# Performance work log

Hardware: AMD Instinct MI355X
Metric: run time of the kernel (lower is better)

## Reference

```python
import jax, jax.numpy as jnp
import numpy as np

B, CIN, COUT, TD, H, W = 32, 128, 128, 192, 64, 64
PH = PW = 8
HEADS, DEPTH, E, K, TASKS = 4, 2, 4, 2, 9
MLPH = int(2.0 * TD)


def _ln(x, g, b, eps=1e-5):
    m = jnp.mean(x, -1, keepdims=True)
    v = jnp.var(x, -1, keepdims=True)
    return (x - m) * jax.lax.rsqrt(v + eps) * g + b


def _conv(x, w):
    return jax.lax.conv_general_dilated(x, w, (1, 1), 'SAME',
        dimension_numbers=('NCHW', 'OIHW', 'NCHW'))


def _bn_act(x, g, b):
    y = g[None, :, None, None] * x + b[None, :, None, None]
    return jax.nn.silu(y)


def setup_inputs() -> dict:
    key = jax.random.key(0)
    ks = iter(jax.random.split(key, 40))
    def nrm(shape, s=0.02):
        return jax.random.normal(next(ks), shape, jnp.float32) * s
    return {
        'x': jax.random.normal(next(ks), (B, CIN, H, W), jnp.float32),
        'w_kxk': nrm((CIN, CIN, 3, 3)), 'bn1_g': jnp.ones((CIN,)), 'bn1_b': jnp.zeros((CIN,)),
        'w_1x1': nrm((TD, CIN)),
        'gate_w': nrm((TASKS, TD, E)),
        'moe_w1': nrm((E, TD, TD)), 'moe_b1': jnp.zeros((E, TD)),
        'moe_w2': nrm((E, TD, TD)), 'moe_b2': jnp.zeros((E, TD)),
        'ln1_g': jnp.ones((DEPTH, TD)), 'ln1_b': jnp.zeros((DEPTH, TD)),
        'qkv_w': nrm((DEPTH, TD, 3 * TD)), 'qkv_b': jnp.zeros((DEPTH, 3 * TD)),
        'proj_w': nrm((DEPTH, TD, TD)), 'proj_b': jnp.zeros((DEPTH, TD)),
        'ln2_g': jnp.ones((DEPTH, TD)), 'ln2_b': jnp.zeros((DEPTH, TD)),
        'fc1_w': nrm((DEPTH, TD, MLPH)), 'fc1_b': jnp.zeros((DEPTH, MLPH)),
        'fc2_w': nrm((DEPTH, MLPH, TD)), 'fc2_b': jnp.zeros((DEPTH, TD)),
        'nrm_g': jnp.ones((TD,)), 'nrm_b': jnp.zeros((TD,)),
        'w_proj': nrm((COUT, TD)), 'bn2_g': jnp.ones((COUT,)), 'bn2_b': jnp.zeros((COUT,)),
        'w_fus': nrm((COUT, CIN + COUT, 3, 3)), 'bn3_g': jnp.ones((COUT,)), 'bn3_b': jnp.zeros((COUT,)),
        'task_bh': 3,
    }


def reference(x, w_kxk, bn1_g, bn1_b, w_1x1, gate_w, moe_w1, moe_b1, moe_w2, moe_b2,
              ln1_g, ln1_b, qkv_w, qkv_b, proj_w, proj_b, ln2_g, ln2_b,
              fc1_w, fc1_b, fc2_w, fc2_b, nrm_g, nrm_b,
              w_proj, bn2_g, bn2_b, w_fus, bn3_g, bn3_b, task_bh):
    shortcut = x
    h = _bn_act(_conv(x, w_kxk), bn1_g, bn1_b)              # conv_kxk + BN + SiLU
    h = jnp.einsum('bchw,tc->bthw', h, w_1x1)               # conv_1x1 (no bias)
    Bh, C, Hh, Wh = h.shape                                 # C == TD
    nph, npw = Hh // PH, Wh // PW
    NP, PA = nph * npw, PH * PW
    # patchify: [B,C,H,W] -> [B*PA, NP, C]
    t = h.reshape(Bh * C * nph, PH, npw, PW)
    t = jnp.swapaxes(t, 1, 2).reshape(Bh, C, NP, PA)
    t = jnp.swapaxes(t, 1, 3).reshape(Bh * PA, NP, C)
    # TaskMoE: task-conditioned top-k routing
    N, S, D = t.shape
    tok = t.reshape(N * S, D)
    logits = tok @ gate_w[task_bh]                          # [T,E]
    probs = jax.nn.softmax(logits, -1)
    topv, topi = jax.lax.top_k(probs, K)
    gates = topv / jnp.sum(topv, -1, keepdims=True)
    dense = jnp.zeros_like(probs)
    for j in range(K):
        dense = dense + jax.nn.one_hot(topi[:, j], E, dtype=probs.dtype) * gates[:, j:j + 1]
    out = jnp.zeros_like(tok)
    for e in range(E):
        he = jax.nn.gelu(tok @ moe_w1[e] + moe_b1[e], approximate=False)
        out = out + dense[:, e:e + 1] * (he @ moe_w2[e] + moe_b2[e])
    importance = jnp.mean(probs, 0)
    load = jnp.mean((dense > 0).astype(probs.dtype), 0)
    moe_loss = E * jnp.sum(importance * load)
    t = out.reshape(N, S, D)
    # transformer blocks
    hd = D // HEADS
    scale = hd ** -0.5
    for l in range(DEPTH):
        y = _ln(t, ln1_g[l], ln1_b[l])
        qkv = (y @ qkv_w[l] + qkv_b[l]).reshape(N, S, 3, HEADS, hd)
        q, k_, v = qkv[:, :, 0], qkv[:, :, 1], qkv[:, :, 2]
        att = jax.nn.softmax(jnp.einsum('nqhd,nkhd->nhqk', q, k_) * scale, -1)
        y = jnp.einsum('nhqk,nkhd->nqhd', att, v).reshape(N, S, D)
        t = t + (y @ proj_w[l] + proj_b[l])
        y = _ln(t, ln2_g[l], ln2_b[l])
        y = jax.nn.gelu(y @ fc1_w[l] + fc1_b[l], approximate=False)
        t = t + (y @ fc2_w[l] + fc2_b[l])
    t = _ln(t, nrm_g, nrm_b)
    # unpatchify: [B*PA, NP, D] -> [B, D, H, W]
    u = t.reshape(Bh, PA, NP, D)
    u = jnp.swapaxes(u, 1, 3).reshape(Bh * D * nph, npw, PH, PW)
    u = jnp.swapaxes(u, 1, 2).reshape(Bh, D, nph * PH, npw * PW)
    p = _bn_act(jnp.einsum('bchw,oc->bohw', u, w_proj), bn2_g, bn2_b)  # conv_proj
    f = _bn_act(_conv(jnp.concatenate([shortcut, p], 1), w_fus), bn3_g, bn3_b)
    return (f, moe_loss)
```

## Files before the change

kernel.cpp:

```cpp
#include <hip/hip_runtime.h>
#include <hip/hip_bf16.h>
#include <cmath>

typedef __hip_bfloat16 bf16;
typedef __attribute__((ext_vector_type(8))) short short8;
typedef __attribute__((ext_vector_type(4))) float float4v;

__device__ __forceinline__ float b2f(bf16 v) { return __bfloat162float(v); }
__device__ __forceinline__ bf16  f2b(float v) { return __float2bfloat16(v); }
__device__ __forceinline__ float bfr(unsigned int u) { union { float f; unsigned int i; } c; c.i = u << 16; return c.f; }
__device__ __forceinline__ void ld4(const float* p, float* o) {
    float4 q = *(const float4*)p; o[0]=q.x; o[1]=q.y; o[2]=q.z; o[3]=q.w;
}
__device__ __forceinline__ void ld4(const bf16* p, float* o) {
    const uint2 q = *(const uint2*)p;
    o[0] = bfr(q.x & 0xffffu); o[1] = bfr(q.x >> 16);
    o[2] = bfr(q.y & 0xffffu); o[3] = bfr(q.y >> 16);
}
template <typename T>
__device__ __forceinline__ void ld8(const T* p, float* o) { ld4(p, o); ld4(p + 4, o + 4); }
__device__ __forceinline__ float ldv(const float* p) { return *p; }
__device__ __forceinline__ float ldv(const bf16* p)  { return b2f(*p); }
__device__ __forceinline__ void  stv(float* p, float v) { *p = v; }
__device__ __forceinline__ void  stv(bf16* p, float v)  { *p = f2b(v); }

__device__ __forceinline__ float siluf(float x) { return x / (1.f + expf(-x)); }
__device__ __forceinline__ float geluf(float x) { return 0.5f * x * (1.f + erff(x * 0.70710678118654752f)); }

__global__ __launch_bounds__(256) void k_prep(
    const float* __restrict__ src, bf16* __restrict__ dst, int K, int N, int nmat)
{
    const int per = K * N;
    const int total = per * nmat;
    const int NT = N >> 4;
    for (int idx = blockIdx.x * 256 + threadIdx.x; idx < total; idx += gridDim.x * 256) {
        int m = idx / per;
        int rem = idx - m * per;
        int k = rem / N, n = rem - k * N;
        int off = ((k >> 5) * NT + (n >> 4)) * 512 + (((k >> 3) & 3) * 16 + (n & 15)) * 8 + (k & 7);
        dst[(size_t)m * per + off] = f2b(src[idx]);
    }
}

__global__ __launch_bounds__(256) void k_prep_t(
    const float* __restrict__ src, bf16* __restrict__ dst, int N, int K)
{
    const int total = N * K;
    const int NT = N >> 4;
    for (int idx = blockIdx.x * 256 + threadIdx.x; idx < total; idx += gridDim.x * 256) {
        int n = idx / K, k = idx - n * K;
        int off = ((k >> 5) * NT + (n >> 4)) * 512 + (((k >> 3) & 3) * 16 + (n & 15)) * 8 + (k & 7);
        dst[off] = f2b(src[idx]);
    }
}

__global__ __launch_bounds__(256) void k_prep_conv(
    const float* __restrict__ src, bf16* __restrict__ dst, int Cin, int Cout)
{
    const int total = Cout * Cin * 9;
    const int NT = Cout >> 4;
    for (int idx = blockIdx.x * 256 + threadIdx.x; idx < total; idx += gridDim.x * 256) {
        int oc = idx / (Cin * 9);
        int rem = idx - oc * (Cin * 9);
        int ic = rem / 9, tap = rem - ic * 9;
        int off = tap * (Cin * Cout)
                + ((ic >> 5) * NT + (oc >> 4)) * 512
                + (((ic >> 3) & 3) * 16 + (oc & 15)) * 8 + (ic & 7);
        dst[off] = f2b(src[idx]);
    }
}

__global__ __launch_bounds__(256) void k_tohwc(const float* __restrict__ x, bf16* __restrict__ xh)
{
    __shared__ bf16 L[64][136];
    const int br = blockIdx.x;
    const int b = br >> 6, y = br & 63;
    for (int idx = threadIdx.x; idx < 8192; idx += 256) {
        int ch = idx >> 6, xc = idx & 63;
        L[xc][ch] = f2b(x[(((size_t)b * 128 + ch) * 64 + y) * 64 + xc]);
    }
    __syncthreads();
    for (int idx = threadIdx.x; idx < 1024; idx += 256) {
        int px = idx >> 4, q = idx & 15;
        *(short8*)(void*)(xh + ((size_t)br * 64 + px) * 128 + q * 8) =
            *(const short8*)(const void*)(&L[px][q * 8]);
    }
}

__global__ __launch_bounds__(256) void k_conv1_mfma(
    const bf16* __restrict__ xh, const bf16* __restrict__ wf,
    const float* __restrict__ gamma, const float* __restrict__ beta,
    bf16* __restrict__ h1h)
{
    __shared__ __align__(16) bf16 outL[64][136];
    const int br = blockIdx.x;
    const int b = br >> 6, y = br & 63;
    const int lane = threadIdx.x & 63, w = threadIdx.x >> 6;
    const int m0 = w * 16, kg = lane >> 4, ln16 = lane & 15;
    float4v acc[8];
    #pragma unroll
    for (int i = 0; i < 8; ++i) acc[i] = (float4v)0.f;
    #pragma unroll
    for (int tap = 0; tap < 9; ++tap) {
        const int ky = tap / 3 - 1, kx = tap % 3 - 1;
        const int yy = y + ky;
        if (yy < 0 || yy > 63) continue;
        const int px = m0 + ln16 + kx;
        const bool valid = (px >= 0) && (px < 64);
        const bf16* wt = wf + tap * 16384;
        #pragma unroll
        for (int kc = 0; kc < 4; ++kc) {
            short8 a = {0, 0, 0, 0, 0, 0, 0, 0};
            if (valid)
                a = *(const short8*)(const void*)(xh + (((size_t)(b * 64 + yy) * 64 + px) * 128) + kc * 32 + kg * 8);
            const bf16* wb = wt + (kc * 8) * 512 + lane * 8;
            #pragma unroll
            for (int nt = 0; nt < 8; ++nt) {
                short8 bfrag = *(const short8*)(const void*)(wb + nt * 512);
                acc[nt] = __builtin_amdgcn_mfma_f32_16x16x32_bf16(a, bfrag, acc[nt], 0, 0, 0);
            }
        }
    }
    #pragma unroll
    for (int nt = 0; nt < 8; ++nt) {
        int c = nt * 16 + ln16;
        float g = gamma[c], be = beta[c];
        #pragma unroll
        for (int r = 0; r < 4; ++r)
            outL[m0 + kg * 4 + r][c] = f2b(siluf(g * acc[nt][r] + be));
    }
    __syncthreads();
    for (int idx = threadIdx.x; idx < 1024; idx += 256) {
        int px = idx >> 4, q = idx & 15;
        *(short8*)(void*)(h1h + ((size_t)br * 64 + px) * 128 + q * 8) =
            *(const short8*)(const void*)(&outL[px][q * 8]);
    }
}

__global__ __launch_bounds__(256) void k_convf_mfma(
    const bf16* __restrict__ xh, const bf16* __restrict__ ph,
    const bf16* __restrict__ wf,
    const float* __restrict__ gamma, const float* __restrict__ beta,
    float* __restrict__ out)
{
    __shared__ float outF[64][129];
    const int br = blockIdx.x;
    const int b = br >> 6, y = br & 63;
    const int lane = threadIdx.x & 63, w = threadIdx.x >> 6;
    const int m0 = w * 16, kg = lane >> 4, ln16 = lane & 15;
    float4v acc[8];
    #pragma unroll
    for (int i = 0; i < 8; ++i) acc[i] = (float4v)0.f;
    #pragma unroll
    for (int tap = 0; tap < 9; ++tap) {
        const int ky = tap / 3 - 1, kx = tap % 3 - 1;
        const int yy = y + ky;
        if (yy < 0 || yy > 63) continue;
        const int px = m0 + ln16 + kx;
        const bool valid = (px >= 0) && (px < 64);
        const size_t rowoff = ((size_t)(b * 64 + yy) * 64 + px) * 128;
        const bf16* wt = wf + tap * 32768;
        #pragma unroll
        for (int kc = 0; kc < 8; ++kc) {
            const bf16* src = (kc < 4) ? xh : ph;
            short8 a = {0, 0, 0, 0, 0, 0, 0, 0};
            if (valid)
                a = *(const short8*)(const void*)(src + rowoff + (kc & 3) * 32 + kg * 8);
            const bf16* wb = wt + (kc * 8) * 512 + lane * 8;
            #pragma unroll
            for (int nt = 0; nt < 8; ++nt) {
                short8 bfrag = *(const short8*)(const void*)(wb + nt * 512);
                acc[nt] = __builtin_amdgcn_mfma_f32_16x16x32_bf16(a, bfrag, acc[nt], 0, 0, 0);
            }
        }
    }
    #pragma unroll
    for (int nt = 0; nt < 8; ++nt) {
        int c = nt * 16 + ln16;
        float g = gamma[c], be = beta[c];
        #pragma unroll
        for (int r = 0; r < 4; ++r)
            outF[m0 + kg * 4 + r][c] = siluf(g * acc[nt][r] + be);
    }
    __syncthreads();
    for (int idx = threadIdx.x; idx < 8192; idx += 256) {
        int oc = idx >> 6, xcol = idx & 63;
        out[(((size_t)b * 128 + oc) * 64 + y) * 64 + xcol] = outF[xcol][oc];
    }
}

template <typename TT>
__global__ __launch_bounds__(512) void k_patchmoe(
    const bf16* __restrict__ h1h, const bf16* __restrict__ w1x1f,
    const float* __restrict__ gate_w_all, const int* __restrict__ task,
    const bf16* __restrict__ w1f, const float* __restrict__ b1,
    const bf16* __restrict__ w2f, const float* __restrict__ b2,
    TT* __restrict__ t, float* __restrict__ part)
{
    __shared__ __align__(16) bf16 outL[64][200];
    __shared__ __align__(16) bf16 hL[2][64][200];
    __shared__ bf16 gwL[768];
    __shared__ float dsm[64][4];
    __shared__ float sm[4][8];
    const int br = blockIdx.x;
    const int b = br >> 6, y = br & 63;
    const int tid = threadIdx.x;
    const int lane = tid & 63;
    const int wv = tid >> 6;
    const int wr = wv & 3, wc = wv >> 2;
    const int kg = lane >> 4, ln16 = lane & 15;
    const int pab = (y & 7) * 8, npb = (y >> 3) * 8;

    for (int i = tid; i < 768; i += 512) gwL[i] = f2b(gate_w_all[(size_t)task[0] * 768 + i]);

    {
        const int m0 = wr * 16;
        float4v acc[6];
        #pragma unroll
        for (int i = 0; i < 6; ++i) acc[i] = (float4v)0.f;
        #pragma unroll
        for (int kc = 0; kc < 4; ++kc) {
            short8 a = *(const short8*)(const void*)(h1h + ((size_t)br * 64 + m0 + ln16) * 128 + kc * 32 + kg * 8);
            const bf16* wb = w1x1f + (kc * 12 + wc * 6) * 512 + lane * 8;
            #pragma unroll
            for (int nt = 0; nt < 6; ++nt) {
                short8 bfrag = *(const short8*)(const void*)(wb + nt * 512);
                acc[nt] = __builtin_amdgcn_mfma_f32_16x16x32_bf16(a, bfrag, acc[nt], 0, 0, 0);
            }
        }
        #pragma unroll
        for (int nt = 0; nt < 6; ++nt) {
            #pragma unroll
            for (int r = 0; r < 4; ++r)
                outL[m0 + kg * 4 + r][(wc * 6 + nt) * 16 + ln16] = f2b(acc[nt][r]);
        }
    }
    __syncthreads();
    if (tid < 256) {
        const int px = tid >> 2, qg = tid & 3;
        float L0 = 0.f, L1 = 0.f, L2 = 0.f, L3 = 0.f;
        #pragma unroll
        for (int i = 0; i < 48; ++i) {
            int c = qg * 48 + i;
            float xv = b2f(outL[px][c]);
            L0 += xv * b2f(gwL[c*4+0]); L1 += xv * b2f(gwL[c*4+1]);
            L2 += xv * b2f(gwL[c*4+2]); L3 += xv * b2f(gwL[c*4+3]);
        }
        L0 += __shfl_xor(L0, 1); L0 += __shfl_xor(L0, 2);
        L1 += __shfl_xor(L1, 1); L1 += __shfl_xor(L1, 2);
        L2 += __shfl_xor(L2, 1); L2 += __shfl_xor(L2, 2);
        L3 += __shfl_xor(L3, 1); L3 += __shfl_xor(L3, 2);
        float vals[8] = {0.f,0.f,0.f,0.f,0.f,0.f,0.f,0.f};
        if (qg == 0) {
            float m = fmaxf(fmaxf(L0, L1), fmaxf(L2, L3));
            float e0 = expf(L0 - m), e1 = expf(L1 - m), e2 = expf(L2 - m), e3 = expf(L3 - m);
            float s = e0 + e1 + e2 + e3;
            float p[4] = {e0 / s, e1 / s, e2 / s, e3 / s};
            int i1 = 0; float v1 = p[0];
            #pragma unroll
            for (int e = 1; e < 4; ++e) if (p[e] > v1) { v1 = p[e]; i1 = e; }
            int i2 = -1; float v2 = -1.f;
            #pragma unroll
            for (int e = 0; e < 4; ++e) if (e != i1 && p[e] > v2) { v2 = p[e]; i2 = e; }
            float gs = v1 + v2;
            float d[4] = {0.f, 0.f, 0.f, 0.f};
            d[i1] = v1 / gs; d[i2] = v2 / gs;
            dsm[px][0] = d[0]; dsm[px][1] = d[1]; dsm[px][2] = d[2]; dsm[px][3] = d[3];
            vals[0]=p[0]; vals[1]=p[1]; vals[2]=p[2]; vals[3]=p[3];
            vals[4]=d[0]>0.f?1.f:0.f; vals[5]=d[1]>0.f?1.f:0.f;
            vals[6]=d[2]>0.f?1.f:0.f; vals[7]=d[3]>0.f?1.f:0.f;
        }
        #pragma unroll
        for (int off = 32; off; off >>= 1)
            #pragma unroll
            for (int i = 0; i < 8; ++i) vals[i] += __shfl_down(vals[i], off);
        if (lane == 0)
            #pragma unroll
            for (int i = 0; i < 8; ++i) sm[wv][i] = vals[i];
    }
    __syncthreads();
    if (tid < 8)
        part[br * 8 + tid] = sm[0][tid] + sm[1][tid] + sm[2][tid] + sm[3][tid];

    const int m0 = wr * 16;
    float g4[4][4];
    #pragma unroll
    for (int e = 0; e < 4; ++e)
        #pragma unroll
        for (int r = 0; r < 4; ++r)
            g4[e][r] = dsm[m0 + kg * 4 + r][e];

    float4v accT[6];
    #pragma unroll
    for (int i = 0; i < 6; ++i) accT[i] = (float4v)0.f;

    for (int e = 0; e < 4; ++e) {
        float4v acc[6];
        #pragma unroll
        for (int i = 0; i < 6; ++i) acc[i] = (float4v)0.f;
        #pragma unroll
        for (int kc = 0; kc < 6; ++kc) {
            short8 a = *(const short8*)(const void*)(&outL[m0 + ln16][kc * 32 + kg * 8]);
            const bf16* wb = w1f + (size_t)e * 36864 + (kc * 12 + wc * 6) * 512 + lane * 8;
            #pragma unroll
            for (int nt = 0; nt < 6; ++nt) {
                short8 bfrag = *(const short8*)(const void*)(wb + nt * 512);
                acc[nt] = __builtin_amdgcn_mfma_f32_16x16x32_bf16(a, bfrag, acc[nt], 0, 0, 0);
            }
        }
        bf16 (*hb)[200] = hL[e & 1];
        #pragma unroll
        for (int nt = 0; nt < 6; ++nt) {
            int c = (wc * 6 + nt) * 16 + ln16;
            float bias = b1[e * 192 + c];
            #pragma unroll
            for (int r = 0; r < 4; ++r)
                hb[m0 + kg * 4 + r][c] = f2b(geluf(acc[nt][r] + bias) * g4[e][r]);
        }
        __syncthreads();
        #pragma unroll
        for (int kc = 0; kc < 6; ++kc) {
            short8 a2 = *(const short8*)(const void*)(&hb[m0 + ln16][kc * 32 + kg * 8]);
            const bf16* wb = w2f + (size_t)e * 36864 + (kc * 12 + wc * 6) * 512 + lane * 8;
            #pragma unroll
            for (int nt = 0; nt < 6; ++nt) {
                short8 bfrag = *(const short8*)(const void*)(wb + nt * 512);
                accT[nt] = __builtin_amdgcn_mfma_f32_16x16x32_bf16(a2, bfrag, accT[nt], 0, 0, 0);
            }
        }
    }
    #pragma unroll
    for (int nt = 0; nt < 6; ++nt) {
        int c = (wc * 6 + nt) * 16 + ln16;
        #pragma unroll
        for (int r = 0; r < 4; ++r) {
            int px = m0 + kg * 4 + r;
            int tokr = (b * 64 + pab + (px & 7)) * 64 + npb + (px >> 3);
            float v = accT[nt][r];
            #pragma unroll
            for (int e = 0; e < 4; ++e) v += g4[e][r] * b2[e * 192 + c];
            stv(&t[(size_t)tokr * 192 + c], v);
        }
    }
}

template <typename TT>
__global__ __launch_bounds__(256) void k_mlp_mfma(
    TT* __restrict__ t, const float* __restrict__ lg, const float* __restrict__ lb,
    const bf16* __restrict__ w1f, const float* __restrict__ b1,
    const bf16* __restrict__ w2f, const float* __restrict__ b2)
{
    __shared__ __align__(16) bf16 yL[64][200];
    __shared__ __align__(16) bf16 hL[64][200];
    const int rbase = blockIdx.x * 64;
    const int tid = threadIdx.x;
    {
        const int row = tid >> 2, qg = tid & 3;
        float v[48];
        const TT* tr_ = t + (size_t)(rbase + row) * 192 + qg * 48;
        float s = 0.f, sq = 0.f;
        #pragma unroll
        for (int i = 0; i < 12; ++i) {
            float tmp[4]; ld4(tr_ + i * 4, tmp);
            #pragma unroll
            for (int j = 0; j < 4; ++j) { v[i*4+j] = tmp[j]; s += tmp[j]; sq += tmp[j]*tmp[j]; }
        }
        s  += __shfl_xor(s, 1);  s  += __shfl_xor(s, 2);
        sq += __shfl_xor(sq, 1); sq += __shfl_xor(sq, 2);
        float m = s * (1.f/192.f), var = sq * (1.f/192.f) - m*m;
        float rs = rsqrtf(var + 1e-5f);
        #pragma unroll
        for (int i = 0; i < 48; ++i) {
            int d = qg * 48 + i;
            yL[row][d] = f2b((v[i] - m) * rs * lg[d] + lb[d]);
        }
    }
    __syncthreads();
    const int lane = tid & 63, w = tid >> 6;
    const int m0 = w * 16;
    const int kg = lane >> 4, ln16 = lane & 15;
    float4v accT[12];
    #pragma unroll
    for (int i = 0; i < 12; ++i) accT[i] = (float4v)0.f;
    for (int ch = 0; ch < 2; ++ch) {
        float4v acc[12];
        #pragma unroll
        for (int i = 0; i < 12; ++i) acc[i] = (float4v)0.f;
        for (int kc = 0; kc < 6; ++kc) {
            short8 a = *(const short8*)(const void*)(&yL[m0 + ln16][kc * 32 + kg * 8]);
            const bf16* wb = w1f + (size_t)(kc * 24 + ch * 12) * 512 + lane * 8;
            #pragma unroll
            for (int nt = 0; nt < 12; ++nt) {
                short8 bfrag = *(const short8*)(const void*)(wb + nt * 512);
                acc[nt] = __builtin_amdgcn_mfma_f32_16x16x32_bf16(a, bfrag, acc[nt], 0, 0, 0);
            }
        }
        #pragma unroll
        for (int nt = 0; nt < 12; ++nt) {
            int c = nt * 16 + ln16;
            float bias = b1[ch * 192 + c];
            #pragma unroll
            for (int r = 0; r < 4; ++r)
                hL[m0 + kg * 4 + r][c] = f2b(geluf(acc[nt][r] + bias));
        }
        __syncthreads();
        for (int kc = 0; kc < 6; ++kc) {
            short8 a = *(const short8*)(const void*)(&hL[m0 + ln16][kc * 32 + kg * 8]);
            const bf16* wb = w2f + (size_t)((ch * 6 + kc) * 12) * 512 + lane * 8;
            #pragma unroll
            for (int nt = 0; nt < 12; ++nt) {
                short8 bfrag = *(const short8*)(const void*)(wb + nt * 512);
                accT[nt] = __builtin_amdgcn_mfma_f32_16x16x32_bf16(a, bfrag, accT[nt], 0, 0, 0);
            }
        }
        __syncthreads();
    }
    #pragma unroll
    for (int nt = 0; nt < 12; ++nt) {
        int c = nt * 16 + ln16;
        float bias = b2[c];
        #pragma unroll
        for (int r = 0; r < 4; ++r) {
            TT* p = &t[(size_t)(rbase + m0 + kg * 4 + r) * 192 + c];
            stv(p, ldv(p) + accT[nt][r] + bias);
        }
    }
}

template <typename TT>
__global__ __launch_bounds__(256) void k_attn_mfma(
    TT* __restrict__ t, const float* __restrict__ lg, const float* __restrict__ lb,
    const bf16* __restrict__ qkvwf, const float* __restrict__ qkvb,
    const bf16* __restrict__ pwf, const float* __restrict__ pb)
{
    __shared__ __align__(16) bf16 smem[39424];
    bf16* Qs = smem;
    bf16* Ks = smem + 12800;
    bf16* vT = smem + 25600;
    bf16* pL = smem;
    bf16* y2L = smem + 25600;
    const int n = blockIdx.x;
    const int tid = threadIdx.x;
    const int w = tid >> 6, lane = tid & 63;
    const int kg = lane >> 4, ln16 = lane & 15;
    const int row = w * 16 + ln16;
    const short8 zfrag = {0, 0, 0, 0, 0, 0, 0, 0};

    short8 afr[6];
    {
        float v[48];
        float s = 0.f, sq = 0.f;
        const TT* tp = t + (size_t)n * 12288 + row * 192 + kg * 8;
        #pragma unroll
        for (int c = 0; c < 6; ++c) {
            float tmp[8]; ld8(tp + c * 32, tmp);
            #pragma unroll
            for (int j = 0; j < 8; ++j) { v[c*8+j] = tmp[j]; s += tmp[j]; sq += tmp[j]*tmp[j]; }
        }
        s  += __shfl_xor(s, 16);  s  += __shfl_xor(s, 32);
        sq += __shfl_xor(sq, 16); sq += __shfl_xor(sq, 32);
        float m = s * (1.f/192.f), var = sq * (1.f/192.f) - m * m;
        float rs = rsqrtf(var + 1e-5f);
        #pragma unroll
        for (int c = 0; c < 6; ++c) {
            float g8[8], b8[8];
            ld8(lg + kg * 8 + c * 32, g8);
            ld8(lb + kg * 8 + c * 32, b8);
            bf16 pk[8];
            #pragma unroll
            for (int j = 0; j < 8; ++j)
                pk[j] = f2b((v[c*8+j] - m) * rs * g8[j] + b8[j]);
            afr[c] = *(const short8*)(const void*)pk;
        }
    }

    const float qscale = 0.14433756729740644f;
    for (int nt = 0; nt < 36; ++nt) {
        float4v acc = (float4v)0.f;
        const bf16* wb = qkvwf + nt * 512 + lane * 8;
        #pragma unroll
        for (int kc = 0; kc < 6; ++kc) {
            short8 bfrag = *(const short8*)(const void*)(wb + kc * 36 * 512);
            acc = __builtin_amdgcn_mfma_f32_16x16x32_bf16(afr[kc], bfrag, acc, 0, 0, 0);
        }
        const int which = nt / 12, h = (nt % 12) / 3, dt = nt % 3;
        const int d = dt * 16 + ln16;
        const float bias = qkvb[nt * 16 + ln16];
        if (which == 0) {
            #pragma unroll
            for (int r = 0; r < 4; ++r)
                Qs[(w * 16 + kg * 4 + r) * 200 + h * 48 + d] = f2b((acc[r] + bias) * qscale);
        } else if (which == 1) {
            #pragma unroll
            for (int r = 0; r < 4; ++r)
                Ks[(w * 16 + kg * 4 + r) * 200 + h * 48 + d] = f2b(acc[r] + bias);
        } else {
            #pragma unroll
            for (int r = 0; r < 4; ++r)
                vT[h * 3456 + d * 72 + (w * 16 + kg * 4 + r)] = f2b(acc[r] + bias);
        }
    }
    __syncthreads();

    float4v sacc[4][4];
    #pragma unroll
    for (int mt = 0; mt < 4; ++mt)
        #pragma unroll
        for (int nt = 0; nt < 4; ++nt) sacc[mt][nt] = (float4v)0.f;
    #pragma unroll
    for (int kc = 0; kc < 2; ++kc) {
        const bool kv = (kc == 0) || (kg < 2);
        short8 aq[4], bk[4];
        #pragma unroll
        for (int mt = 0; mt < 4; ++mt)
            aq[mt] = kv ? *(const short8*)(const void*)(Qs + (mt * 16 + ln16) * 200 + w * 48 + kc * 32 + kg * 8) : zfrag;
        #pragma unroll
        for (int nt = 0; nt < 4; ++nt)
            bk[nt] = kv ? *(const short8*)(const void*)(Ks + (nt * 16 + ln16) * 200 + w * 48 + kc * 32 + kg * 8) : zfrag;
        #pragma unroll
        for (int mt = 0; mt < 4; ++mt)
            #pragma unroll
            for (int nt = 0; nt < 4; ++nt)
                sacc[mt][nt] = __builtin_amdgcn_mfma_f32_16x16x32_bf16(aq[mt], bk[nt], sacc[mt][nt], 0, 0, 0);
    }
    __syncthreads();

    #pragma unroll
    for (int mt = 0; mt < 4; ++mt) {
        #pragma unroll
        for (int r = 0; r < 4; ++r) {
            float mx = sacc[mt][0][r];
            #pragma unroll
            for (int nt = 1; nt < 4; ++nt) mx = fmaxf(mx, sacc[mt][nt][r]);
            mx = fmaxf(mx, __shfl_xor(mx, 1)); mx = fmaxf(mx, __shfl_xor(mx, 2));
            mx = fmaxf(mx, __shfl_xor(mx, 4)); mx = fmaxf(mx, __shfl_xor(mx, 8));
            float e[4], sum = 0.f;
            #pragma unroll
            for (int nt = 0; nt < 4; ++nt) { e[nt] = expf(sacc[mt][nt][r] - mx); sum += e[nt]; }
            sum += __shfl_xor(sum, 1); sum += __shfl_xor(sum, 2);
            sum += __shfl_xor(sum, 4); sum += __shfl_xor(sum, 8);
            float inv = 1.f / sum;
            #pragma unroll
            for (int nt = 0; nt < 4; ++nt)
                pL[w * 4608 + (mt * 16 + kg * 4 + r) * 72 + nt * 16 + ln16] = f2b(e[nt] * inv);
        }
    }
    float4v oacc[4][3];
    #pragma unroll
    for (int mt = 0; mt < 4; ++mt)
        #pragma unroll
        for (int nt = 0; nt < 3; ++nt) oacc[mt][nt] = (float4v)0.f;
    #pragma unroll
    for (int kc = 0; kc < 2; ++kc) {
        short8 ap[4], bv[3];
        #pragma unroll
        for (int mt = 0; mt < 4; ++mt)
            ap[mt] = *(const short8*)(const void*)(pL + w * 4608 + (mt * 16 + ln16) * 72 + kc * 32 + kg * 8);
        #pragma unroll
        for (int nt = 0; nt < 3; ++nt)
            bv[nt] = *(const short8*)(const void*)(vT + w * 3456 + (nt * 16 + ln16) * 72 + kc * 32 + kg * 8);
        #pragma unroll
        for (int mt = 0; mt < 4; ++mt)
            #pragma unroll
            for (int nt = 0; nt < 3; ++nt)
                oacc[mt][nt] = __builtin_amdgcn_mfma_f32_16x16x32_bf16(ap[mt], bv[nt], oacc[mt][nt], 0, 0, 0);
    }
    __syncthreads();
    #pragma unroll
    for (int mt = 0; mt < 4; ++mt)
        #pragma unroll
        for (int nt = 0; nt < 3; ++nt)
            #pragma unroll
            for (int r = 0; r < 4; ++r)
                y2L[(mt * 16 + kg * 4 + r) * 200 + w * 48 + nt * 16 + ln16] = f2b(oacc[mt][nt][r]);
    __syncthreads();
    float4v pacc[12];
    #pragma unroll
    for (int i = 0; i < 12; ++i) pacc[i] = (float4v)0.f;
    #pragma unroll
    for (int kc = 0; kc < 6; ++kc) {
        short8 a = *(const short8*)(const void*)(y2L + row * 200 + kc * 32 + kg * 8);
        const bf16* wb = pwf + (kc * 12) * 512 + lane * 8;
        #pragma unroll
        for (int nt = 0; nt < 12; ++nt) {
            short8 bfrag = *(const short8*)(const void*)(wb + nt * 512);
            pacc[nt] = __builtin_amdgcn_mfma_f32_16x16x32_bf16(a, bfrag, pacc[nt], 0, 0, 0);
        }
    }
    #pragma unroll
    for (int nt = 0; nt < 12; ++nt) {
        int c = nt * 16 + ln16;
        float bias = pb[c];
        #pragma unroll
        for (int r = 0; r < 4; ++r) {
            TT* p = &t[((size_t)n * 64 + w * 16 + kg * 4 + r) * 192 + c];
            stv(p, ldv(p) + pacc[nt][r] + bias);
        }
    }
}

template <typename TT>
__global__ __launch_bounds__(256) void k_unpatch_mfma(
    const TT* __restrict__ t, const float* __restrict__ ng, const float* __restrict__ nb,
    const bf16* __restrict__ wpf, const float* __restrict__ gamma, const float* __restrict__ beta,
    bf16* __restrict__ ph)
{
    __shared__ __align__(16) bf16 outL[64][136];
    const int blk = blockIdx.x;
    const int b = blk >> 6, pa = blk & 63;
    const int tid = threadIdx.x;
    const int w = tid >> 6, lane = tid & 63;
    const int kg = lane >> 4, ln16 = lane & 15;
    const int row = w * 16 + ln16;

    short8 afr[6];
    {
        float v[48];
        float s = 0.f, sq = 0.f;
        const TT* tp = t + ((size_t)blk * 64 + row) * 192 + kg * 8;
        #pragma unroll
        for (int c = 0; c < 6; ++c) {
            float tmp[8]; ld8(tp + c * 32, tmp);
            #pragma unroll
            for (int j = 0; j < 8; ++j) { v[c*8+j] = tmp[j]; s += tmp[j]; sq += tmp[j]*tmp[j]; }
        }
        s  += __shfl_xor(s, 16);  s  += __shfl_xor(s, 32);
        sq += __shfl_xor(sq, 16); sq += __shfl_xor(sq, 32);
        float m = s * (1.f/192.f), var = sq * (1.f/192.f) - m * m;
        float rs = rsqrtf(var + 1e-5f);
        #pragma unroll
        for (int c = 0; c < 6; ++c) {
            float g8[8], b8[8];
            ld8(ng + kg * 8 + c * 32, g8);
            ld8(nb + kg * 8 + c * 32, b8);
            bf16 pk[8];
            #pragma unroll
            for (int j = 0; j < 8; ++j)
                pk[j] = f2b((v[c*8+j] - m) * rs * g8[j] + b8[j]);
            afr[c] = *(const short8*)(const void*)pk;
        }
    }

    float4v acc[8];
    #pragma unroll
    for (int i = 0; i < 8; ++i) acc[i] = (float4v)0.f;
    #pragma unroll
    for (int kc = 0; kc < 6; ++kc) {
        const bf16* wb = wpf + (kc * 8) * 512 + lane * 8;
        #pragma unroll
        for (int nt = 0; nt < 8; ++nt) {
            short8 bfrag = *(const short8*)(const void*)(wb + nt * 512);
            acc[nt] = __builtin_amdgcn_mfma_f32_16x16x32_bf16(afr[kc], bfrag, acc[nt], 0, 0, 0);
        }
    }
    #pragma unroll
    for (int nt = 0; nt < 8; ++nt) {
        int c = nt * 16 + ln16;
        float g = gamma[c], be = beta[c];
        #pragma unroll
        for (int r = 0; r < 4; ++r)
            outL[w * 16 + kg * 4 + r][c] = f2b(siluf(g * acc[nt][r] + be));
    }
    __syncthreads();
    for (int idx = tid; idx < 1024; idx += 256) {
        int np = idx >> 4, q = idx & 15;
        int yy = (np >> 3) * 8 + (pa >> 3), xx = (np & 7) * 8 + (pa & 7);
        *(short8*)(void*)(ph + ((size_t)(b * 64 + yy) * 64 + xx) * 128 + q * 8) =
            *(const short8*)(const void*)(&outL[np][q * 8]);
    }
}

__global__ __launch_bounds__(256) void k_loss(const float* __restrict__ part, float* __restrict__ out)
{
    __shared__ float red[8][33];
    const int tid = threadIdx.x;
    const int e = tid & 7, g = tid >> 3;
    float s = 0.f;
    for (int i = g; i < 2048; i += 32) s += part[i * 8 + e];
    red[e][g] = s;
    __syncthreads();
    if (tid < 8) {
        float t2 = 0.f;
        for (int g2 = 0; g2 < 32; ++g2) t2 += red[tid][g2];
        red[tid][32] = t2;
    }
    __syncthreads();
    if (tid == 0) {
        float L = 0.f;
        for (int e2 = 0; e2 < 4; ++e2)
            L += (red[e2][32] / 131072.f) * (red[4 + e2][32] / 131072.f);
        out[16777216] = 4.f * L;
    }
}

template <typename TT>
static void run_pipeline(const float* x, const float* w_kxk, const float* bn1_g, const float* bn1_b,
                         const float* w_1x1, const float* gate_w,
                         const float* moe_w1, const float* moe_b1, const float* moe_w2, const float* moe_b2,
                         const float* ln1_g, const float* ln1_b, const float* qkv_w, const float* qkv_b,
                         const float* proj_w, const float* proj_b, const float* ln2_g, const float* ln2_b,
                         const float* fc1_w, const float* fc1_b, const float* fc2_w, const float* fc2_b,
                         const float* nrm_g, const float* nrm_b, const float* w_proj, const float* bn2_g,
                         const float* bn2_b, const float* w_fus, const float* bn3_g, const float* bn3_b,
                         const int* task, float* out, bf16* xh, bf16* tok, TT* t, float* part,
                         bf16* wprep, hipStream_t stream)
{
    bf16* moeW1f = wprep;
    bf16* moeW2f = wprep + 147456;
    bf16* fc1f   = wprep + 294912;
    bf16* fc2f   = wprep + 442368;
    bf16* projWf = wprep + 589824;
    bf16* w1x1f  = wprep + 663552;
    bf16* convW1f= wprep + 688128;
    bf16* convWFf= wprep + 835584;
    bf16* qkvWf  = wprep + 1130496;
    bf16* wpjf   = wprep + 1351680;
    hipLaunchKernelGGL(k_prep, dim3(576), dim3(256), 0, stream, moe_w1, moeW1f, 192, 192, 4);
    hipLaunchKernelGGL(k_prep, dim3(576), dim3(256), 0, stream, moe_w2, moeW2f, 192, 192, 4);
    hipLaunchKernelGGL(k_prep, dim3(576), dim3(256), 0, stream, fc1_w, fc1f, 192, 384, 2);
    hipLaunchKernelGGL(k_prep, dim3(576), dim3(256), 0, stream, fc2_w, fc2f, 384, 192, 2);
    hipLaunchKernelGGL(k_prep, dim3(288), dim3(256), 0, stream, proj_w, projWf, 192, 192, 2);
    hipLaunchKernelGGL(k_prep_t, dim3(96), dim3(256), 0, stream, w_1x1, w1x1f, 192, 128);
    hipLaunchKernelGGL(k_prep_conv, dim3(576), dim3(256), 0, stream, w_kxk, convW1f, 128, 128);
    hipLaunchKernelGGL(k_prep_conv, dim3(1152), dim3(256), 0, stream, w_fus, convWFf, 256, 128);
    hipLaunchKernelGGL(k_prep, dim3(864), dim3(256), 0, stream, qkv_w, qkvWf, 192, 576, 2);
    hipLaunchKernelGGL(k_prep_t, dim3(96), dim3(256), 0, stream, w_proj, wpjf, 128, 192);

    bf16* h1h = (bf16*)out;
    hipLaunchKernelGGL(k_tohwc, dim3(2048), dim3(256), 0, stream, x, xh);
    hipLaunchKernelGGL(k_conv1_mfma, dim3(2048), dim3(256), 0, stream, xh, convW1f, bn1_g, bn1_b, h1h);
    hipLaunchKernelGGL(k_patchmoe<TT>, dim3(2048), dim3(512), 0, stream,
                       h1h, w1x1f, gate_w, task, moeW1f, moe_b1, moeW2f, moe_b2, t, part);
    for (int l = 0; l < 2; ++l) {
        hipLaunchKernelGGL(k_attn_mfma<TT>, dim3(2048), dim3(256), 0, stream,
                           t, ln1_g + l * 192, ln1_b + l * 192,
                           qkvWf + (size_t)l * 110592, qkv_b + l * 576,
                           projWf + (size_t)l * 36864, proj_b + l * 192);
        hipLaunchKernelGGL(k_mlp_mfma<TT>, dim3(2048), dim3(256), 0, stream,
                           t, ln2_g + l * 192, ln2_b + l * 192,
                           fc1f + (size_t)l * 73728, fc1_b + l * 384,
                           fc2f + (size_t)l * 73728, fc2_b + l * 192);
    }
    bf16* ph = tok;
    hipLaunchKernelGGL(k_unpatch_mfma<TT>, dim3(2048), dim3(256), 0, stream,
                       t, nrm_g, nrm_b, wpjf, bn2_g, bn2_b, ph);
    hipLaunchKernelGGL(k_convf_mfma, dim3(2048), dim3(256), 0, stream,
                       xh, ph, convWFf, bn3_g, bn3_b, out);
    hipLaunchKernelGGL(k_loss, dim3(1), dim3(256), 0, stream, part, out);
}

extern "C" void kernel_launch(void* const* d_in, const int* in_sizes, int n_in,
                              void* d_out, int out_size, void* d_ws, size_t ws_size,
                              hipStream_t stream) {
    const float* x      = (const float*)d_in[0];
    const float* w_kxk  = (const float*)d_in[1];
    const float* bn1_g  = (const float*)d_in[2];
    const float* bn1_b  = (const float*)d_in[3];
    const float* w_1x1  = (const float*)d_in[4];
    const float* gate_w = (const float*)d_in[5];
    const float* moe_w1 = (const float*)d_in[6];
    const float* moe_b1 = (const float*)d_in[7];
    const float* moe_w2 = (const float*)d_in[8];
    const float* moe_b2 = (const float*)d_in[9];
    const float* ln1_g  = (const float*)d_in[10];
    const float* ln1_b  = (const float*)d_in[11];
    const float* qkv_w  = (const float*)d_in[12];
    const float* qkv_b  = (const float*)d_in[13];
    const float* proj_w = (const float*)d_in[14];
    const float* proj_b = (const float*)d_in[15];
    const float* ln2_g  = (const float*)d_in[16];
    const float* ln2_b  = (const float*)d_in[17];
    const float* fc1_w  = (const float*)d_in[18];
    const float* fc1_b  = (const float*)d_in[19];
    const float* fc2_w  = (const float*)d_in[20];
    const float* fc2_b  = (const float*)d_in[21];
    const float* nrm_g  = (const float*)d_in[22];
    const float* nrm_b  = (const float*)d_in[23];
    const float* w_proj = (const float*)d_in[24];
    const float* bn2_g  = (const float*)d_in[25];
    const float* bn2_b  = (const float*)d_in[26];
    const float* w_fus  = (const float*)d_in[27];
    const float* bn3_g  = (const float*)d_in[28];
    const float* bn3_b  = (const float*)d_in[29];
    const int*  task    = (const int*)d_in[30];

    char* wsb = (char*)d_ws;
    const size_t XHB   = 33554432ull;
    const size_t TOKB  = 50331648ull;
    const size_t T32B  = 100663296ull;
    const size_t T16B  = 50331648ull;
    const size_t DENB  = 2097152ull;
    const size_t PARB  = 65536ull;
    const size_t WPB   = 2752512ull;
    bf16* xh  = (bf16*)wsb;
    bf16* tok = (bf16*)(wsb + XHB);
    float* out = (float*)d_out;

    if (ws_size >= XHB + TOKB + T32B + DENB + PARB + WPB) {
        float* t     = (float*)(wsb + XHB + TOKB);
        float* part  = (float*)(wsb + XHB + TOKB + T32B + DENB);
        bf16*  wprep = (bf16*)(wsb + XHB + TOKB + T32B + DENB + PARB);
        run_pipeline<float>(x, w_kxk, bn1_g, bn1_b, w_1x1, gate_w, moe_w1, moe_b1, moe_w2, moe_b2,
                            ln1_g, ln1_b, qkv_w, qkv_b, proj_w, proj_b, ln2_g, ln2_b,
                            fc1_w, fc1_b, fc2_w, fc2_b, nrm_g, nrm_b, w_proj, bn2_g, bn2_b,
                            w_fus, bn3_g, bn3_b, task, out, xh, tok, t, part, wprep, stream);
    } else {
        bf16*  t     = (bf16*)(wsb + XHB + TOKB);
        float* part  = (float*)(wsb + XHB + TOKB + T16B + DENB);
        bf16*  wprep = (bf16*)(wsb + XHB + TOKB + T16B + DENB + PARB);
        run_pipeline<bf16>(x, w_kxk, bn1_g, bn1_b, w_1x1, gate_w, moe_w1, moe_b1, moe_w2, moe_b2,
                           ln1_g, ln1_b, qkv_w, qkv_b, proj_w, proj_b, ln2_g, ln2_b,
                           fc1_w, fc1_b, fc2_w, fc2_b, nrm_g, nrm_b, w_proj, bn2_g, bn2_b,
                           w_fus, bn3_g, bn3_b, task, out, xh, tok, t, part, wprep, stream);
    }
}
```

Before: 1.290 ms.

## Fuse MLP block into attention kernel, keeping residual in registers

Merges the MLP kernel into the attention kernel. Both work on the same 64-token block, so the post-attention residual stays in registers and goes straight into LN2 and the fc1/fc2 MFMA GEMMs. This removes one kernel launch per layer and one round trip of the token tensor through global memory. In exchange the fused kernel holds more live registers (the tn array plus accumulators), which could lower occupancy or cause spills.

```diff
diff --git a/kernel.cpp b/kernel.cpp
--- a/kernel.cpp
+++ b/kernel.cpp
@@ -345,93 +345,13 @@
 }
 
 template <typename TT>
-__global__ __launch_bounds__(256) void k_mlp_mfma(
-    TT* __restrict__ t, const float* __restrict__ lg, const float* __restrict__ lb,
-    const bf16* __restrict__ w1f, const float* __restrict__ b1,
-    const bf16* __restrict__ w2f, const float* __restrict__ b2)
-{
-    __shared__ __align__(16) bf16 yL[64][200];
-    __shared__ __align__(16) bf16 hL[64][200];
-    const int rbase = blockIdx.x * 64;
-    const int tid = threadIdx.x;
-    {
-        const int row = tid >> 2, qg = tid & 3;
-        float v[48];
-        const TT* tr_ = t + (size_t)(rbase + row) * 192 + qg * 48;
-        float s = 0.f, sq = 0.f;
-        #pragma unroll
-        for (int i = 0; i < 12; ++i) {
-            float tmp[4]; ld4(tr_ + i * 4, tmp);
-            #pragma unroll
-            for (int j = 0; j < 4; ++j) { v[i*4+j] = tmp[j]; s += tmp[j]; sq += tmp[j]*tmp[j]; }
-        }
-        s  += __shfl_xor(s, 1);  s  += __shfl_xor(s, 2);
-        sq += __shfl_xor(sq, 1); sq += __shfl_xor(sq, 2);
-        float m = s * (1.f/192.f), var = sq * (1.f/192.f) - m*m;
-        float rs = rsqrtf(var + 1e-5f);
-        #pragma unroll
-        for (int i = 0; i < 48; ++i) {
-            int d = qg * 48 + i;
-            yL[row][d] = f2b((v[i] - m) * rs * lg[d] + lb[d]);
-        }
-    }
-    __syncthreads();
-    const int lane = tid & 63, w = tid >> 6;
-    const int m0 = w * 16;
-    const int kg = lane >> 4, ln16 = lane & 15;
-    float4v accT[12];
-    #pragma unroll
-    for (int i = 0; i < 12; ++i) accT[i] = (float4v)0.f;
-    for (int ch = 0; ch < 2; ++ch) {
-        float4v acc[12];
-        #pragma unroll
-        for (int i = 0; i < 12; ++i) acc[i] = (float4v)0.f;
-        for (int kc = 0; kc < 6; ++kc) {
-            short8 a = *(const short8*)(const void*)(&yL[m0 + ln16][kc * 32 + kg * 8]);
-            const bf16* wb = w1f + (size_t)(kc * 24 + ch * 12) * 512 + lane * 8;
-            #pragma unroll
-            for (int nt = 0; nt < 12; ++nt) {
-                short8 bfrag = *(const short8*)(const void*)(wb + nt * 512);
-                acc[nt] = __builtin_amdgcn_mfma_f32_16x16x32_bf16(a, bfrag, acc[nt], 0, 0, 0);
-            }
-        }
-        #pragma unroll
-        for (int nt = 0; nt < 12; ++nt) {
-            int c = nt * 16 + ln16;
-            float bias = b1[ch * 192 + c];
-            #pragma unroll
-            for (int r = 0; r < 4; ++r)
-                hL[m0 + kg * 4 + r][c] = f2b(geluf(acc[nt][r] + bias));
-        }
-        __syncthreads();
-        for (int kc = 0; kc < 6; ++kc) {
-            short8 a = *(const short8*)(const void*)(&hL[m0 + ln16][kc * 32 + kg * 8]);
-            const bf16* wb = w2f + (size_t)((ch * 6 + kc) * 12) * 512 + lane * 8;
-            #pragma unroll
-            for (int nt = 0; nt < 12; ++nt) {
-                short8 bfrag = *(const short8*)(const void*)(wb + nt * 512);
-                accT[nt] = __builtin_amdgcn_mfma_f32_16x16x32_bf16(a, bfrag, accT[nt], 0, 0, 0);
-            }
-        }
-        __syncthreads();
-    }
-    #pragma unroll
-    for (int nt = 0; nt < 12; ++nt) {
-        int c = nt * 16 + ln16;
-        float bias = b2[c];
-        #pragma unroll
-        for (int r = 0; r < 4; ++r) {
-            TT* p = &t[(size_t)(rbase + m0 + kg * 4 + r) * 192 + c];
-            stv(p, ldv(p) + accT[nt][r] + bias);
-        }
-    }
-}
-
-template <typename TT>
-__global__ __launch_bounds__(256) void k_attn_mfma(
+__global__ __launch_bounds__(256) void k_attnmlp(
     TT* __restrict__ t, const float* __restrict__ lg, const float* __restrict__ lb,
     const bf16* __restrict__ qkvwf, const float* __restrict__ qkvb,
-    const bf16* __restrict__ pwf, const float* __restrict__ pb)
+    const bf16* __restrict__ pwf, const float* __restrict__ pb,
+    const float* __restrict__ lg2, const float* __restrict__ lb2,
+    const bf16* __restrict__ fw1f, const float* __restrict__ fb1,
+    const bf16* __restrict__ fw2f, const float* __restrict__ fb2)
 {
     __shared__ __align__(16) bf16 smem[39424];
     bf16* Qs = smem;
@@ -439,6 +359,8 @@
     bf16* vT = smem + 25600;
     bf16* pL = smem;
     bf16* y2L = smem + 25600;
+    bf16* yL = smem;
+    bf16* hM = smem + 12800;
     const int n = blockIdx.x;
     const int tid = threadIdx.x;
     const int w = tid >> 6, lane = tid & 63;
@@ -587,15 +509,91 @@
             pacc[nt] = __builtin_amdgcn_mfma_f32_16x16x32_bf16(a, bfrag, pacc[nt], 0, 0, 0);
         }
     }
+    float tn[12][4];
     #pragma unroll
     for (int nt = 0; nt < 12; ++nt) {
         int c = nt * 16 + ln16;
         float bias = pb[c];
         #pragma unroll
+        for (int r = 0; r < 4; ++r)
+            tn[nt][r] = ldv(&t[((size_t)n * 64 + w * 16 + kg * 4 + r) * 192 + c]) + pacc[nt][r] + bias;
+    }
+    float srow[4] = {0.f,0.f,0.f,0.f}, sqrow[4] = {0.f,0.f,0.f,0.f};
+    #pragma unroll
+    for (int nt = 0; nt < 12; ++nt)
+        #pragma unroll
+        for (int r = 0; r < 4; ++r) { float v = tn[nt][r]; srow[r] += v; sqrow[r] += v * v; }
+    #pragma unroll
+    for (int msk = 1; msk <= 8; msk <<= 1) {
+        #pragma unroll
         for (int r = 0; r < 4; ++r) {
-            TT* p = &t[((size_t)n * 64 + w * 16 + kg * 4 + r) * 192 + c];
-            stv(p, ldv(p) + pacc[nt][r] + bias);
-        }
+            srow[r]  += __shfl_xor(srow[r], msk);
+            sqrow[r] += __shfl_xor(sqrow[r], msk);
+        }
+    }
+    float meanr[4], rsr[4];
+    #pragma unroll
+    for (int r = 0; r < 4; ++r) {
+        meanr[r] = srow[r] * (1.f/192.f);
+        float var = sqrow[r] * (1.f/192.f) - meanr[r] * meanr[r];
+        rsr[r] = rsqrtf(var + 1e-5f);
+    }
+    __syncthreads();
+    #pragma unroll
+    for (int nt = 0; nt < 12; ++nt) {
+        int c = nt * 16 + ln16;
+        float g2 = lg2[c], bb2 = lb2[c];
+        #pragma unroll
+        for (int r = 0; r < 4; ++r)
+            yL[(w * 16 + kg * 4 + r) * 200 + c] = f2b((tn[nt][r] - meanr[r]) * rsr[r] * g2 + bb2);
+    }
+    __syncthreads();
+    float4v accM[12];
+    #pragma unroll
+    for (int i = 0; i < 12; ++i) accM[i] = (float4v)0.f;
+    for (int ch = 0; ch < 2; ++ch) {
+        float4v acc1[12];
+        #pragma unroll
+        for (int i = 0; i < 12; ++i) acc1[i] = (float4v)0.f;
+        #pragma unroll
+        for (int kc = 0; kc < 6; ++kc) {
+            short8 a = *(const short8*)(const void*)(yL + row * 200 + kc * 32 + kg * 8);
+            const bf16* wb = fw1f + (size_t)(kc * 24 + ch * 12) * 512 + lane * 8;
+            #pragma unroll
+            for (int nt = 0; nt < 12; ++nt) {
+                short8 bfrag = *(const short8*)(const void*)(wb + nt * 512);
+                acc1[nt] = __builtin_amdgcn_mfma_f32_16x16x32_bf16(a, bfrag, acc1[nt], 0, 0, 0);
+            }
+        }
+        #pragma unroll
+        for (int nt = 0; nt < 12; ++nt) {
+            int c = nt * 16 + ln16;
+            float bias = fb1[ch * 192 + c];
+            #pragma unroll
+            for (int r = 0; r < 4; ++r)
+                hM[(w * 16 + kg * 4 + r) * 200 + c] = f2b(geluf(acc1[nt][r] + bias));
+        }
+        __syncthreads();
+        #pragma unroll
+        for (int kc = 0; kc < 6; ++kc) {
+            short8 a2 = *(const short8*)(const void*)(hM + row * 200 + kc * 32 + kg * 8);
+            const bf16* wb = fw2f + (size_t)((ch * 6 + kc) * 12) * 512 + lane * 8;
+            #pragma unroll
+            for (int nt = 0; nt < 12; ++nt) {
+                short8 bfrag = *(const short8*)(const void*)(wb + nt * 512);
+                accM[nt] = __builtin_amdgcn_mfma_f32_16x16x32_bf16(a2, bfrag, accM[nt], 0, 0, 0);
+            }
+        }
+        __syncthreads();
+    }
+    #pragma unroll
+    for (int nt = 0; nt < 12; ++nt) {
+        int c = nt * 16 + ln16;
+        float bias = fb2[c];
+        #pragma unroll
+        for (int r = 0; r < 4; ++r)
+            stv(&t[((size_t)n * 64 + w * 16 + kg * 4 + r) * 192 + c],
+                tn[nt][r] + accM[nt][r] + bias);
     }
 }
 
@@ -732,12 +730,11 @@
     hipLaunchKernelGGL(k_patchmoe<TT>, dim3(2048), dim3(512), 0, stream,
                        h1h, w1x1f, gate_w, task, moeW1f, moe_b1, moeW2f, moe_b2, t, part);
     for (int l = 0; l < 2; ++l) {
-        hipLaunchKernelGGL(k_attn_mfma<TT>, dim3(2048), dim3(256), 0, stream,
+        hipLaunchKernelGGL(k_attnmlp<TT>, dim3(2048), dim3(256), 0, stream,
                            t, ln1_g + l * 192, ln1_b + l * 192,
                            qkvWf + (size_t)l * 110592, qkv_b + l * 576,
-                           projWf + (size_t)l * 36864, proj_b + l * 192);
-        hipLaunchKernelGGL(k_mlp_mfma<TT>, dim3(2048), dim3(256), 0, stream,
-                           t, ln2_g + l * 192, ln2_b + l * 192,
+                           projWf + (size_t)l * 36864, proj_b + l * 192,
+                           ln2_g + l * 192, ln2_b + l * 192,
                            fc1f + (size_t)l * 73728, fc1_b + l * 384,
                            fc2f + (size_t)l * 73728, fc2_b + l * 192);
     }
```

After: 1.750 ms. +35.7%, slower.
